# Optimization experiments

Measured on AMD Instinct MI355X. Metric: run time of the kernel, lower is better.

## Reference

```python
import jax, jax.numpy as jnp
import numpy as np

N_USERS = 100000
N_ITEMS = 50000
N_NODES = 50000
N_EDGES = 1600000
B = 16384
H, D = 4, 32  # num_heads, out_feats per head
D_IMG, D_TXT, D_AUD = 1024, 768, 128
EMB = 128
SLOPE = 0.2


def setup_inputs() -> dict:
    key = jax.random.key(0)
    ks = jax.random.split(key, 40)
    s = 0.02

    def n(i, shape, scale=s):
        return jax.random.normal(ks[i], shape, jnp.float32) * scale

    inp = {
        "user_ids": jax.random.randint(ks[0], (B,), 0, N_USERS, jnp.int32),
        "item_ids": jax.random.randint(ks[1], (B,), 0, N_ITEMS, jnp.int32),
        "src": jax.random.randint(ks[2], (N_EDGES,), 0, N_NODES, jnp.int32),
        "dst": jax.random.randint(ks[3], (N_EDGES,), 0, N_NODES, jnp.int32),
        "feat_image": jax.random.normal(ks[4], (N_NODES, D_IMG), jnp.float32),
        "feat_text": jax.random.normal(ks[5], (N_NODES, D_TXT), jnp.float32),
        "feat_audio": jax.random.normal(ks[6], (N_NODES, D_AUD), jnp.float32),
        # embedding tables
        "user_table": n(7, (N_USERS, EMB)),
        "item_table": n(8, (N_ITEMS, EMB)),
        # modality transforms (Linear: y = x @ W.T + b)
        "Wi": n(9, (32, D_IMG)), "bi": n(10, (32,)),
        "Wt": n(11, (32, D_TXT)), "bt": n(12, (32,)),
        "Wa": n(13, (32, D_AUD)), "ba": n(14, (32,)),
        # GAT params per modality: fc weight [H*D, 32], attn vectors [H, D], output bias [H*D]
        "gWi": n(15, (H * D, 32), 0.1), "ali": n(16, (H, D), 0.1), "ari": n(17, (H, D), 0.1), "gbi": n(18, (H * D,)),
        "gWt": n(19, (H * D, 32), 0.1), "alt": n(20, (H, D), 0.1), "art": n(21, (H, D), 0.1), "gbt": n(22, (H * D,)),
        "gWa": n(23, (H * D, 32), 0.1), "ala": n(24, (H, D), 0.1), "ara": n(25, (H, D), 0.1), "gba": n(26, (H * D,)),
        # final fc: Linear(32*3*H=384 -> 128)
        "fcW": n(27, (EMB, 3 * H * D)), "fcb": n(28, (EMB,)),
    }
    return inp


def _gat(x, W, al, ar, b, src, dst):
    """DGL GATConv: fc -> per-head additive attention -> edge softmax over dst -> sum."""
    h = (x @ W.T).reshape(N_NODES, H, D)                      # [N,H,D]
    el = jnp.einsum('nhd,hd->nh', h, al)                      # [N,H]
    er = jnp.einsum('nhd,hd->nh', h, ar)                      # [N,H]
    e = jax.nn.leaky_relu(el[src] + er[dst], SLOPE)           # [E,H]
    emax = jax.ops.segment_max(e, dst, num_segments=N_NODES)  # [N,H] (-inf for empty, unused)
    a = jnp.exp(e - emax[dst])                                # [E,H]
    denom = jax.ops.segment_sum(a, dst, num_segments=N_NODES)
    a = a / jnp.maximum(denom[dst], 1e-9)
    msg = a[:, :, None] * h[src]                              # [E,H,D]
    out = jax.ops.segment_sum(msg, dst, num_segments=N_NODES) # [N,H,D]
    return (out + b.reshape(1, H, D)).reshape(N_NODES, H * D)


def reference(user_ids, item_ids, src, dst, feat_image, feat_text, feat_audio,
              user_table, item_table, Wi, bi, Wt, bt, Wa, ba,
              gWi, ali, ari, gbi, gWt, alt, art, gbt, gWa, ala, ara, gba,
              fcW, fcb):
    user_emb = user_table[user_ids]
    item_emb = item_table[item_ids]
    xi = jax.nn.relu(feat_image @ Wi.T + bi)
    xt = jax.nn.relu(feat_text @ Wt.T + bt)
    xa = jax.nn.relu(feat_audio @ Wa.T + ba)
    gi = _gat(xi, gWi, ali, ari, gbi, src, dst)
    gt = _gat(xt, gWt, alt, art, gbt, src, dst)
    ga = _gat(xa, gWa, ala, ara, gba, src, dst)
    comb = jnp.concatenate([gi, gt, ga], axis=1)              # [N, 3*H*D]
    comb = jax.nn.relu(comb @ fcW.T + fcb)                    # [N, 128]
    return (user_emb, item_emb, comb)
```

## Files before the change

### kernel.cpp

```cpp
#include <hip/hip_runtime.h>
#include <stdint.h>

#define NNODES 50000
#define NEDGES 1600000
#define NB     16384
#define HD     128
#define COMBW  384

typedef unsigned short u16;
typedef __bf16 bf16x8 __attribute__((ext_vector_type(8)));
typedef float  f32x4  __attribute__((ext_vector_type(4)));

__device__ __forceinline__ float b2f(u16 u){
    union { unsigned int i; float f; } v; v.i = ((unsigned int)u) << 16; return v.f;
}
__device__ __forceinline__ u16 f2b(float f){
    union { float f; unsigned int i; } v; v.f = f;
    unsigned int x = v.i;
    unsigned int r = (x + 0x7fffu + ((x >> 16) & 1u)) >> 16;
    return (u16)r;
}
__device__ __forceinline__ bf16x8 pack8(const float* __restrict__ p){
    uint4 a = *(const uint4*)p;
    uint4 b = *(const uint4*)(p + 4);
    union { u16 s[8]; bf16x8 v; } u;
    u.s[0] = (u16)(a.x >> 16); u.s[1] = (u16)(a.y >> 16);
    u.s[2] = (u16)(a.z >> 16); u.s[3] = (u16)(a.w >> 16);
    u.s[4] = (u16)(b.x >> 16); u.s[5] = (u16)(b.y >> 16);
    u.s[6] = (u16)(b.z >> 16); u.s[7] = (u16)(b.w >> 16);
    return u.v;
}

__global__ void k_gather(const int* __restrict__ uid, const int* __restrict__ iid,
                         const float* __restrict__ utab, const float* __restrict__ itab,
                         float* __restrict__ out){
    int i = blockIdx.x * blockDim.x + threadIdx.x;
    const int total = 2 * NB * HD / 8;
    if (i >= total) return;
    int e8 = i * 8;
    const float* p;
    if (e8 < NB * HD) {
        int row = e8 >> 7, c = e8 & 127;
        p = utab + (size_t)uid[row] * HD + c;
    } else {
        int e2 = e8 - NB * HD;
        int row = e2 >> 7, c = e2 & 127;
        p = itab + (size_t)iid[row] * HD + c;
    }
    *(uint4*)(out + e8)     = *(const uint4*)p;
    *(uint4*)(out + e8 + 4) = *(const uint4*)(p + 4);
}

__global__ __launch_bounds__(256) void k_feat(const float* __restrict__ feat, int K,
                                              const float* __restrict__ W,
                                              const float* __restrict__ bias,
                                              float* __restrict__ xout){
    int wave = threadIdx.x >> 6, lane = threadIdx.x & 63;
    int quad = lane >> 4, m = lane & 15;
    int row0 = blockIdx.x * 64 + wave * 16;
    int arow = row0 + m; if (arow >= NNODES) arow = NNODES - 1;
    const float* ap  = feat + (size_t)arow * K + quad * 8;
    const float* bp0 = W + (size_t)m        * K + quad * 8;
    const float* bp1 = W + (size_t)(m + 16) * K + quad * 8;
    f32x4 c0 = {0.f,0.f,0.f,0.f}, c1 = {0.f,0.f,0.f,0.f};
    for (int k = 0; k < K; k += 32){
        bf16x8 a  = pack8(ap  + k);
        bf16x8 b0 = pack8(bp0 + k);
        bf16x8 b1 = pack8(bp1 + k);
        c0 = __builtin_amdgcn_mfma_f32_16x16x32_bf16(a, b0, c0, 0, 0, 0);
        c1 = __builtin_amdgcn_mfma_f32_16x16x32_bf16(a, b1, c1, 0, 0, 0);
    }
    float bv0 = bias[m], bv1 = bias[m + 16];
    #pragma unroll
    for (int i = 0; i < 4; i++){
        int r = row0 + quad * 4 + i;
        if (r < NNODES){
            float v0 = c0[i] + bv0; v0 = v0 > 0.f ? v0 : 0.f;
            float v1 = c1[i] + bv1; v1 = v1 > 0.f ? v1 : 0.f;
            xout[(size_t)r * 32 + m]      = v0;
            xout[(size_t)r * 32 + m + 16] = v1;
        }
    }
}

__global__ __launch_bounds__(256) void k_node(const float* __restrict__ x,
                                              const float* __restrict__ gW,
                                              const float* __restrict__ al,
                                              const float* __restrict__ ar,
                                              u16* __restrict__ hout,
                                              float* __restrict__ el,
                                              float* __restrict__ er){
    int head = blockIdx.y;
    int n = blockIdx.x * blockDim.x + threadIdx.x;
    int nc = n < NNODES ? n : NNODES - 1;
    float xr[32];
    const float4* xp = (const float4*)(x + (size_t)nc * 32);
    #pragma unroll
    for (int i = 0; i < 8; i++){
        float4 v = xp[i];
        xr[4*i] = v.x; xr[4*i+1] = v.y; xr[4*i+2] = v.z; xr[4*i+3] = v.w;
    }
    const float* wbase = gW + head * 1024;
    const float* alh = al + head * 32;
    const float* arh = ar + head * 32;
    u16* hp = hout + (size_t)nc * COMBW + head * 32;
    float elv = 0.f, erv = 0.f;
    #pragma unroll
    for (int cg = 0; cg < 4; cg++){
        float acc[8];
        #pragma unroll
        for (int c = 0; c < 8; c++){
            const float* wr = wbase + (cg * 8 + c) * 32;
            float a = 0.f;
            #pragma unroll
            for (int k = 0; k < 32; k++) a += xr[k] * wr[k];
            acc[c] = a;
            elv += a * alh[cg * 8 + c];
            erv += a * arh[cg * 8 + c];
        }
        union { u16 s[8]; uint4 q; } u;
        #pragma unroll
        for (int c = 0; c < 8; c++) u.s[c] = f2b(acc[c]);
        *(uint4*)(hp + cg * 8) = u.q;
    }
    el[(size_t)nc * 4 + head] = elv;
    er[(size_t)nc * 4 + head] = erv;
}

__global__ void k_hist(const int* __restrict__ dst, int* __restrict__ cnt){
    int i = blockIdx.x * blockDim.x + threadIdx.x;
    if (i < NEDGES) atomicAdd(&cnt[dst[i]], 1);
}

__global__ __launch_bounds__(1024) void k_scan(const int* __restrict__ cnt, int* __restrict__ rp){
    __shared__ int wsum[16];
    int t = threadIdx.x, lane = t & 63, w = t >> 6;
    int carry = 0;
    for (int base = 0; base < NNODES; base += 1024){
        int v = (base + t < NNODES) ? cnt[base + t] : 0;
        int x = v;
        #pragma unroll
        for (int off = 1; off < 64; off <<= 1){
            int u = __shfl_up(x, off, 64);
            if (lane >= off) x += u;
        }
        if (lane == 63) wsum[w] = x;
        __syncthreads();
        if (w == 0){
            int s = (lane < 16) ? wsum[lane] : 0;
            #pragma unroll
            for (int off = 1; off < 16; off <<= 1){
                int u = __shfl_up(s, off, 64);
                if (lane >= off) s += u;
            }
            if (lane < 16) wsum[lane] = s;
        }
        __syncthreads();
        int woff = (w > 0) ? wsum[w - 1] : 0;
        if (base + t < NNODES) rp[base + t] = carry + woff + x - v;
        carry += wsum[15];
        __syncthreads();
    }
    if (t == 0) rp[NNODES] = carry;
}

template<int WITHW>
__global__ __launch_bounds__(256) void k_scatter(const int* __restrict__ src, const int* __restrict__ dst,
                          const int* __restrict__ rp, int* __restrict__ fill,
                          int* __restrict__ col,
                          const float* __restrict__ el0, const float* __restrict__ er0,
                          const float* __restrict__ el1, const float* __restrict__ er1,
                          const float* __restrict__ el2, const float* __restrict__ er2,
                          float* __restrict__ w){
    int i = blockIdx.x * blockDim.x + threadIdx.x;
    if (i >= NEDGES) return;
    int s = src[i], d = dst[i];
    int p = rp[d] + atomicAdd(&fill[d], 1);
    col[p] = s;
    if (WITHW){
        float4 l0 = *(const float4*)(el0 + (size_t)s * 4);
        float4 r0 = *(const float4*)(er0 + (size_t)d * 4);
        float4 l1 = *(const float4*)(el1 + (size_t)s * 4);
        float4 r1 = *(const float4*)(er1 + (size_t)d * 4);
        float4 l2 = *(const float4*)(el2 + (size_t)s * 4);
        float4 r2 = *(const float4*)(er2 + (size_t)d * 4);
        float4 w0, w1, w2;
        #define LKEXP(a, b) __expf(fmaxf((a) + (b), 0.2f * ((a) + (b))))
        w0.x = LKEXP(l0.x, r0.x); w0.y = LKEXP(l0.y, r0.y); w0.z = LKEXP(l0.z, r0.z); w0.w = LKEXP(l0.w, r0.w);
        w1.x = LKEXP(l1.x, r1.x); w1.y = LKEXP(l1.y, r1.y); w1.z = LKEXP(l1.z, r1.z); w1.w = LKEXP(l1.w, r1.w);
        w2.x = LKEXP(l2.x, r2.x); w2.y = LKEXP(l2.y, r2.y); w2.z = LKEXP(l2.z, r2.z); w2.w = LKEXP(l2.w, r2.w);
        #undef LKEXP
        float4* wp = (float4*)(w + (size_t)p * 12);
        wp[0] = w0; wp[1] = w1; wp[2] = w2;
    }
}

template<int PRE>
__global__ __launch_bounds__(128) void k_gat(
        const int* __restrict__ rp, const int* __restrict__ col,
        const u16* __restrict__ hcat, const float* __restrict__ w,
        const float* __restrict__ el0, const float* __restrict__ er0,
        const float* __restrict__ el1, const float* __restrict__ er1,
        const float* __restrict__ el2, const float* __restrict__ er2,
        const float* __restrict__ gb0, const float* __restrict__ gb1, const float* __restrict__ gb2,
        u16* __restrict__ comb){
    int n = blockIdx.x, t = threadIdx.x;
    int head = t >> 5;
    float a0 = 0.f, a1 = 0.f, a2 = 0.f, d0 = 0.f, d1 = 0.f, d2 = 0.f;
    int beg = rp[n], end = rp[n + 1];
    if (PRE){
        const float* wp = w + (size_t)beg * 12 + head;
        for (int e = beg; e < end; e++, wp += 12){
            int s = col[e];
            const u16* hp = hcat + (size_t)s * COMBW + t;
            float w0 = wp[0], w1 = wp[4], w2 = wp[8];
            a0 += w0 * b2f(hp[0]);   d0 += w0;
            a1 += w1 * b2f(hp[128]); d1 += w1;
            a2 += w2 * b2f(hp[256]); d2 += w2;
        }
    } else {
        float e0 = er0[(size_t)n * 4 + head];
        float e1 = er1[(size_t)n * 4 + head];
        float e2 = er2[(size_t)n * 4 + head];
        for (int e = beg; e < end; e++){
            int s = col[e];
            const u16* hp = hcat + (size_t)s * COMBW + t;
            float v0 = el0[(size_t)s * 4 + head] + e0; v0 = fmaxf(v0, 0.2f * v0);
            float v1 = el1[(size_t)s * 4 + head] + e1; v1 = fmaxf(v1, 0.2f * v1);
            float v2 = el2[(size_t)s * 4 + head] + e2; v2 = fmaxf(v2, 0.2f * v2);
            float w0 = __expf(v0), w1 = __expf(v1), w2 = __expf(v2);
            a0 += w0 * b2f(hp[0]);   d0 += w0;
            a1 += w1 * b2f(hp[128]); d1 += w1;
            a2 += w2 * b2f(hp[256]); d2 += w2;
        }
    }
    size_t o = (size_t)n * COMBW;
    comb[o + t]       = f2b(a0 / fmaxf(d0, 1e-9f) + gb0[t]);
    comb[o + 128 + t] = f2b(a1 / fmaxf(d1, 1e-9f) + gb1[t]);
    comb[o + 256 + t] = f2b(a2 / fmaxf(d2, 1e-9f) + gb2[t]);
}

__global__ __launch_bounds__(256) void k_fc(const u16* __restrict__ comb,
                                            const float* __restrict__ fcW,
                                            const float* __restrict__ fcb,
                                            float* __restrict__ out){
    int wave = threadIdx.x >> 6, lane = threadIdx.x & 63;
    int quad = lane >> 4, m = lane & 15;
    int row0 = blockIdx.x * 64 + wave * 16;
    int arow = row0 + m; if (arow >= NNODES) arow = NNODES - 1;
    const u16* ap = comb + (size_t)arow * COMBW + quad * 8;
    f32x4 c[8];
    #pragma unroll
    for (int f = 0; f < 8; f++) c[f] = (f32x4){0.f,0.f,0.f,0.f};
    for (int k = 0; k < COMBW; k += 32){
        bf16x8 a = *(const bf16x8*)(ap + k);
        #pragma unroll
        for (int f = 0; f < 8; f++){
            bf16x8 b = pack8(fcW + (size_t)(f * 16 + m) * COMBW + k + quad * 8);
            c[f] = __builtin_amdgcn_mfma_f32_16x16x32_bf16(a, b, c[f], 0, 0, 0);
        }
    }
    #pragma unroll
    for (int f = 0; f < 8; f++){
        int colc = f * 16 + m;
        float bv = fcb[colc];
        #pragma unroll
        for (int i = 0; i < 4; i++){
            int r = row0 + quad * 4 + i;
            if (r < NNODES){
                float v = c[f][i] + bv; v = v > 0.f ? v : 0.f;
                out[(size_t)(2 * NB * HD) + (size_t)r * HD + colc] = v;
            }
        }
    }
}

extern "C" void kernel_launch(void* const* d_in, const int* in_sizes, int n_in,
                              void* d_out, int out_size, void* d_ws, size_t ws_size,
                              hipStream_t stream){
    const int* uid = (const int*)d_in[0];
    const int* iid = (const int*)d_in[1];
    const int* src = (const int*)d_in[2];
    const int* dst = (const int*)d_in[3];
    const float* fimg = (const float*)d_in[4];
    const float* ftxt = (const float*)d_in[5];
    const float* faud = (const float*)d_in[6];
    const float* utab = (const float*)d_in[7];
    const float* itab = (const float*)d_in[8];
    const float* Wi = (const float*)d_in[9],  *bi = (const float*)d_in[10];
    const float* Wt = (const float*)d_in[11], *bt = (const float*)d_in[12];
    const float* Wa = (const float*)d_in[13], *ba = (const float*)d_in[14];
    const float* gWi = (const float*)d_in[15], *ali = (const float*)d_in[16],
               *ari = (const float*)d_in[17], *gbi = (const float*)d_in[18];
    const float* gWt = (const float*)d_in[19], *alt = (const float*)d_in[20],
               *art = (const float*)d_in[21], *gbt = (const float*)d_in[22];
    const float* gWa = (const float*)d_in[23], *ala = (const float*)d_in[24],
               *ara = (const float*)d_in[25], *gba = (const float*)d_in[26];
    const float* fcW = (const float*)d_in[27], *fcb = (const float*)d_in[28];
    float* out = (float*)d_out;

    char* ws = (char*)d_ws;
    u16*   hcat = (u16*)  (ws + 0);
    u16*   comb = (u16*)  (ws + 38400000);
    float* x    = (float*)(ws + 76800000);
    float* el   = (float*)(ws + 83200000);
    float* er   = (float*)(ws + 85600000);
    int*   cnt  = (int*)  (ws + 88000000);
    int*   fill = (int*)  (ws + 88200000);
    int*   rp   = (int*)  (ws + 88400000);
    int*   col  = (int*)  (ws + 88600064);
    float* w    = (float*)(ws + 95000064);
    const size_t NEED_W = 95000064u + (size_t)NEDGES * 12 * sizeof(float);

    float* el0 = el,           *el1 = el + 200000, *el2 = el + 400000;
    float* er0 = er,           *er1 = er + 200000, *er2 = er + 400000;

    hipMemsetAsync(cnt, 0, 400000, stream);

    k_hist<<<(NEDGES + 255) / 256, 256, 0, stream>>>(dst, cnt);
    k_scan<<<1, 1024, 0, stream>>>(cnt, rp);

    k_gather<<<(2 * NB * HD / 8 + 255) / 256, 256, 0, stream>>>(uid, iid, utab, itab, out);

    dim3 ngrid((NNODES + 255) / 256, 4);
    k_feat<<<(NNODES + 63) / 64, 256, 0, stream>>>(fimg, 1024, Wi, bi, x);
    k_node<<<ngrid, 256, 0, stream>>>(x, gWi, ali, ari, hcat,       el0, er0);
    k_feat<<<(NNODES + 63) / 64, 256, 0, stream>>>(ftxt, 768, Wt, bt, x);
    k_node<<<ngrid, 256, 0, stream>>>(x, gWt, alt, art, hcat + 128, el1, er1);
    k_feat<<<(NNODES + 63) / 64, 256, 0, stream>>>(faud, 128, Wa, ba, x);
    k_node<<<ngrid, 256, 0, stream>>>(x, gWa, ala, ara, hcat + 256, el2, er2);

    if (ws_size >= NEED_W){
        k_scatter<1><<<(NEDGES + 255) / 256, 256, 0, stream>>>(src, dst, rp, fill, col,
                                                               el0, er0, el1, er1, el2, er2, w);
        k_gat<1><<<NNODES, 128, 0, stream>>>(rp, col, hcat, w,
                                             el0, er0, el1, er1, el2, er2,
                                             gbi, gbt, gba, comb);
    } else {
        k_scatter<0><<<(NEDGES + 255) / 256, 256, 0, stream>>>(src, dst, rp, fill, col,
                                                               el0, er0, el1, er1, el2, er2, w);
        k_gat<0><<<NNODES, 128, 0, stream>>>(rp, col, hcat, w,
                                             el0, er0, el1, er1, el2, er2,
                                             gbi, gbt, gba, comb);
    }

    k_fc<<<(NNODES + 63) / 64, 256, 0, stream>>>(comb, fcW, fcb, out);
}
```

Before: 1.190 ms.

## Parallelize CSR scan across blocks and widen GAT aggregation to 384 threads

```diff
diff --git a/kernel.cpp b/kernel.cpp
--- a/kernel.cpp
+++ b/kernel.cpp
@@ -6,6 +6,7 @@
 #define NB     16384
 #define HD     128
 #define COMBW  384
+#define SCAN_BLOCKS ((NNODES + 255) / 256)
 
 typedef unsigned short u16;
 typedef __bf16 bf16x8 __attribute__((ext_vector_type(8)));
@@ -132,36 +133,56 @@
     if (i < NEDGES) atomicAdd(&cnt[dst[i]], 1);
 }
 
-__global__ __launch_bounds__(1024) void k_scan(const int* __restrict__ cnt, int* __restrict__ rp){
-    __shared__ int wsum[16];
+__global__ __launch_bounds__(256) void k_scan1(const int* __restrict__ cnt,
+                                               int* __restrict__ rp,
+                                               int* __restrict__ bsum){
+    __shared__ int ws[4];
     int t = threadIdx.x, lane = t & 63, w = t >> 6;
-    int carry = 0;
-    for (int base = 0; base < NNODES; base += 1024){
-        int v = (base + t < NNODES) ? cnt[base + t] : 0;
-        int x = v;
-        #pragma unroll
-        for (int off = 1; off < 64; off <<= 1){
-            int u = __shfl_up(x, off, 64);
-            if (lane >= off) x += u;
-        }
-        if (lane == 63) wsum[w] = x;
-        __syncthreads();
-        if (w == 0){
-            int s = (lane < 16) ? wsum[lane] : 0;
-            #pragma unroll
-            for (int off = 1; off < 16; off <<= 1){
-                int u = __shfl_up(s, off, 64);
-                if (lane >= off) s += u;
-            }
-            if (lane < 16) wsum[lane] = s;
-        }
-        __syncthreads();
-        int woff = (w > 0) ? wsum[w - 1] : 0;
-        if (base + t < NNODES) rp[base + t] = carry + woff + x - v;
-        carry += wsum[15];
-        __syncthreads();
-    }
-    if (t == 0) rp[NNODES] = carry;
+    int i = blockIdx.x * 256 + t;
+    int v = (i < NNODES) ? cnt[i] : 0;
+    int x = v;
+    #pragma unroll
+    for (int off = 1; off < 64; off <<= 1){
+        int u = __shfl_up(x, off, 64);
+        if (lane >= off) x += u;
+    }
+    if (lane == 63) ws[w] = x;
+    __syncthreads();
+    if (t == 0){
+        int s = 0;
+        #pragma unroll
+        for (int j = 0; j < 4; j++){ int tmp = ws[j]; ws[j] = s; s += tmp; }
+        bsum[blockIdx.x] = s;
+    }
+    __syncthreads();
+    if (i < NNODES) rp[i] = ws[w] + x - v;
+}
+
+__global__ __launch_bounds__(256) void k_scan2(int* __restrict__ bsum, int* __restrict__ rp){
+    __shared__ int ws[4];
+    int t = threadIdx.x, lane = t & 63, w = t >> 6;
+    int v = (t < SCAN_BLOCKS) ? bsum[t] : 0;
+    int x = v;
+    #pragma unroll
+    for (int off = 1; off < 64; off <<= 1){
+        int u = __shfl_up(x, off, 64);
+        if (lane >= off) x += u;
+    }
+    if (lane == 63) ws[w] = x;
+    __syncthreads();
+    if (t == 0){
+        int s = 0;
+        #pragma unroll
+        for (int j = 0; j < 4; j++){ int tmp = ws[j]; ws[j] = s; s += tmp; }
+        rp[NNODES] = s;
+    }
+    __syncthreads();
+    if (t < SCAN_BLOCKS) bsum[t] = ws[w] + x - v;
+}
+
+__global__ __launch_bounds__(256) void k_scan3(int* __restrict__ rp, const int* __restrict__ bsum){
+    int i = blockIdx.x * 256 + threadIdx.x;
+    if (i < NNODES) rp[i] += bsum[blockIdx.x];
 }
 
 template<int WITHW>
@@ -195,10 +216,45 @@
     }
 }
 
-template<int PRE>
-__global__ __launch_bounds__(128) void k_gat(
+__global__ __launch_bounds__(384) void k_gat(
         const int* __restrict__ rp, const int* __restrict__ col,
         const u16* __restrict__ hcat, const float* __restrict__ w,
+        const float* __restrict__ gb0, const float* __restrict__ gb1, const float* __restrict__ gb2,
+        u16* __restrict__ comb){
+    int n = blockIdx.x, t = threadIdx.x;
+    int mod = t >> 7;
+    int head = (t >> 5) & 3;
+    int beg = rp[n], end = rp[n + 1];
+    float acc = 0.f, dsum = 0.f;
+    const float* wp = w + (size_t)beg * 12 + mod * 4 + head;
+    const u16* hbase = hcat + t;
+    int e = beg;
+    for (; e + 4 <= end; e += 4){
+        int s0 = col[e], s1 = col[e + 1], s2 = col[e + 2], s3 = col[e + 3];
+        float w0 = wp[0], w1 = wp[12], w2 = wp[24], w3 = wp[36];
+        wp += 48;
+        float h0 = b2f(hbase[(size_t)s0 * COMBW]);
+        float h1 = b2f(hbase[(size_t)s1 * COMBW]);
+        float h2 = b2f(hbase[(size_t)s2 * COMBW]);
+        float h3 = b2f(hbase[(size_t)s3 * COMBW]);
+        acc += w0 * h0; dsum += w0;
+        acc += w1 * h1; dsum += w1;
+        acc += w2 * h2; dsum += w2;
+        acc += w3 * h3; dsum += w3;
+    }
+    for (; e < end; e++, wp += 12){
+        int s = col[e];
+        float wv = wp[0];
+        acc += wv * b2f(hbase[(size_t)s * COMBW]);
+        dsum += wv;
+    }
+    const float* gb = (mod == 0) ? gb0 : ((mod == 1) ? gb1 : gb2);
+    comb[(size_t)n * COMBW + t] = f2b(acc / fmaxf(dsum, 1e-9f) + gb[t & 127]);
+}
+
+__global__ __launch_bounds__(128) void k_gat_fb(
+        const int* __restrict__ rp, const int* __restrict__ col,
+        const u16* __restrict__ hcat,
         const float* __restrict__ el0, const float* __restrict__ er0,
         const float* __restrict__ el1, const float* __restrict__ er1,
         const float* __restrict__ el2, const float* __restrict__ er2,
@@ -208,31 +264,19 @@
     int head = t >> 5;
     float a0 = 0.f, a1 = 0.f, a2 = 0.f, d0 = 0.f, d1 = 0.f, d2 = 0.f;
     int beg = rp[n], end = rp[n + 1];
-    if (PRE){
-        const float* wp = w + (size_t)beg * 12 + head;
-        for (int e = beg; e < end; e++, wp += 12){
-            int s = col[e];
-            const u16* hp = hcat + (size_t)s * COMBW + t;
-            float w0 = wp[0], w1 = wp[4], w2 = wp[8];
-            a0 += w0 * b2f(hp[0]);   d0 += w0;
-            a1 += w1 * b2f(hp[128]); d1 += w1;
-            a2 += w2 * b2f(hp[256]); d2 += w2;
-        }
-    } else {
-        float e0 = er0[(size_t)n * 4 + head];
-        float e1 = er1[(size_t)n * 4 + head];
-        float e2 = er2[(size_t)n * 4 + head];
-        for (int e = beg; e < end; e++){
-            int s = col[e];
-            const u16* hp = hcat + (size_t)s * COMBW + t;
-            float v0 = el0[(size_t)s * 4 + head] + e0; v0 = fmaxf(v0, 0.2f * v0);
-            float v1 = el1[(size_t)s * 4 + head] + e1; v1 = fmaxf(v1, 0.2f * v1);
-            float v2 = el2[(size_t)s * 4 + head] + e2; v2 = fmaxf(v2, 0.2f * v2);
-            float w0 = __expf(v0), w1 = __expf(v1), w2 = __expf(v2);
-            a0 += w0 * b2f(hp[0]);   d0 += w0;
-            a1 += w1 * b2f(hp[128]); d1 += w1;
-            a2 += w2 * b2f(hp[256]); d2 += w2;
-        }
+    float e0 = er0[(size_t)n * 4 + head];
+    float e1 = er1[(size_t)n * 4 + head];
+    float e2 = er2[(size_t)n * 4 + head];
+    for (int e = beg; e < end; e++){
+        int s = col[e];
+        const u16* hp = hcat + (size_t)s * COMBW + t;
+        float v0 = el0[(size_t)s * 4 + head] + e0; v0 = fmaxf(v0, 0.2f * v0);
+        float v1 = el1[(size_t)s * 4 + head] + e1; v1 = fmaxf(v1, 0.2f * v1);
+        float v2 = el2[(size_t)s * 4 + head] + e2; v2 = fmaxf(v2, 0.2f * v2);
+        float w0 = __expf(v0), w1 = __expf(v1), w2 = __expf(v2);
+        a0 += w0 * b2f(hp[0]);   d0 += w0;
+        a1 += w1 * b2f(hp[128]); d1 += w1;
+        a2 += w2 * b2f(hp[256]); d2 += w2;
     }
     size_t o = (size_t)n * COMBW;
     comb[o + t]       = f2b(a0 / fmaxf(d0, 1e-9f) + gb0[t]);
@@ -311,6 +355,7 @@
     int*   col  = (int*)  (ws + 88600064);
     float* w    = (float*)(ws + 95000064);
     const size_t NEED_W = 95000064u + (size_t)NEDGES * 12 * sizeof(float);
+    int*   bsum = (int*)x;
 
     float* el0 = el,           *el1 = el + 200000, *el2 = el + 400000;
     float* er0 = er,           *er1 = er + 200000, *er2 = er + 400000;
@@ -318,7 +363,9 @@
     hipMemsetAsync(cnt, 0, 400000, stream);
 
     k_hist<<<(NEDGES + 255) / 256, 256, 0, stream>>>(dst, cnt);
-    k_scan<<<1, 1024, 0, stream>>>(cnt, rp);
+    k_scan1<<<SCAN_BLOCKS, 256, 0, stream>>>(cnt, rp, bsum);
+    k_scan2<<<1, 256, 0, stream>>>(bsum, rp);
+    k_scan3<<<SCAN_BLOCKS, 256, 0, stream>>>(rp, bsum);
 
     k_gather<<<(2 * NB * HD / 8 + 255) / 256, 256, 0, stream>>>(uid, iid, utab, itab, out);
 
@@ -333,13 +380,11 @@
     if (ws_size >= NEED_W){
         k_scatter<1><<<(NEDGES + 255) / 256, 256, 0, stream>>>(src, dst, rp, fill, col,
                                                                el0, er0, el1, er1, el2, er2, w);
-        k_gat<1><<<NNODES, 128, 0, stream>>>(rp, col, hcat, w,
-                                             el0, er0, el1, er1, el2, er2,
-                                             gbi, gbt, gba, comb);
+        k_gat<<<NNODES, 384, 0, stream>>>(rp, col, hcat, w, gbi, gbt, gba, comb);
     } else {
         k_scatter<0><<<(NEDGES + 255) / 256, 256, 0, stream>>>(src, dst, rp, fill, col,
                                                                el0, er0, el1, er1, el2, er2, w);
-        k_gat<0><<<NNODES, 128, 0, stream>>>(rp, col, hcat, w,
+        k_gat_fb<<<NNODES, 128, 0, stream>>>(rp, col, hcat,
                                              el0, er0, el1, er1, el2, er2,
                                              gbi, gbt, gba, comb);
     }
```

Result: slower. 1.217 ms (+2.2%).
